# Performance work log

Hardware: AMD Instinct MI355X
Metric: run time of the kernel (lower is better)

## Reference

```python
import jax, jax.numpy as jnp
import numpy as np

MACRO_CURVE_ORDER = 3
MAX_ACTION_LEN = 24
NUM_CURVES = 8
VOCAB = 361
NUM_LAYERS = 6
HID = 32


def setup_inputs() -> dict:
    key = jax.random.key(0)
    ks = iter(jax.random.split(key, 32))
    B, N_PART, P, CTX = 4096, 100, 64, 64

    def lin(k, din, dout):
        k1, k2 = jax.random.split(k)
        s = 1.0 / np.sqrt(din)
        return (jax.random.uniform(k1, (din, dout), jnp.float32, -s, s),
                jax.random.uniform(k2, (dout,), jnp.float32, -s, s))

    fc1_w, fc1_b = lin(next(ks), P, 256)
    fc2_w, fc2_b = lin(next(ks), 256, 256)
    fc3_w, fc3_b = lin(next(ks), CTX + 256, 512)
    fc4_w, fc4_b = lin(next(ks), 512, 256)
    fc5_w, fc5_b = lin(next(ks), 256, 128)
    fc6_w, fc6_b = lin(next(ks), 128, 32)
    fc10_w, fc10_b = lin(next(ks), HID, VOCAB)

    s = 1.0 / np.sqrt(HID)
    lstm_wih = jax.random.uniform(next(ks), (NUM_LAYERS, HID, 4 * HID), jnp.float32, -s, s)
    lstm_whh = jax.random.uniform(next(ks), (NUM_LAYERS, HID, 4 * HID), jnp.float32, -s, s)
    lstm_bih = jax.random.uniform(next(ks), (NUM_LAYERS, 4 * HID), jnp.float32, -s, s)
    lstm_bhh = jax.random.uniform(next(ks), (NUM_LAYERS, 4 * HID), jnp.float32, -s, s)

    return {
        "c": jax.random.normal(next(ks), (B, CTX), jnp.float32),
        "x": jax.random.normal(next(ks), (B, N_PART * P), jnp.float32),
        "hidden": jnp.zeros((NUM_LAYERS, B, HID), jnp.float32),
        "cell": jnp.zeros((NUM_LAYERS, B, HID), jnp.float32),
        "fc1_w": fc1_w, "fc1_b": fc1_b, "fc2_w": fc2_w, "fc2_b": fc2_b,
        "fc3_w": fc3_w, "fc3_b": fc3_b, "fc4_w": fc4_w, "fc4_b": fc4_b,
        "fc5_w": fc5_w, "fc5_b": fc5_b, "fc6_w": fc6_w, "fc6_b": fc6_b,
        "lstm_wih": lstm_wih, "lstm_whh": lstm_whh,
        "lstm_bih": lstm_bih, "lstm_bhh": lstm_bhh,
        "fc10_w": fc10_w, "fc10_b": fc10_b,
        "particle_size": P,
    }


def _lstm_stack(x, h, c, wih, whh, bih, bhh):
    """One time step through 6 stacked LSTM layers (PyTorch cell math)."""
    hs, cs = [], []
    inp = x
    for l in range(NUM_LAYERS):
        gates = inp @ wih[l] + bih[l] + h[l] @ whh[l] + bhh[l]  # (B, 4*HID)
        i, f, g, o = jnp.split(gates, 4, axis=-1)
        i, f, o = jax.nn.sigmoid(i), jax.nn.sigmoid(f), jax.nn.sigmoid(o)
        g = jnp.tanh(g)
        c_new = f * c[l] + i * g
        h_new = o * jnp.tanh(c_new)
        hs.append(h_new)
        cs.append(c_new)
        inp = h_new
    return inp, jnp.stack(hs), jnp.stack(cs)


def reference(c, x, hidden, cell, fc1_w, fc1_b, fc2_w, fc2_b, fc3_w, fc3_b,
              fc4_w, fc4_b, fc5_w, fc5_b, fc6_w, fc6_b,
              lstm_wih, lstm_whh, lstm_bih, lstm_bhh, fc10_w, fc10_b,
              particle_size):
    B = x.shape[0]
    # Belief (particle) encoder with mean pooling.
    xp = x.reshape(B, -1, particle_size)
    xp = jax.nn.relu(xp @ fc1_w + fc1_b)
    xp = jax.nn.relu(xp @ fc2_w + fc2_b)
    xp = xp.mean(axis=-2)  # (B, 256)
    z = jnp.concatenate([c, xp], axis=-1)
    z = jax.nn.relu(z @ fc3_w + fc3_b)
    z = jax.nn.relu(z @ fc4_w + fc4_b)
    z = jax.nn.relu(z @ fc5_w + fc5_b)
    z = jax.nn.relu(z @ fc6_w + fc6_b)  # (B, 32)

    def step(carry, _):
        xt, h, cst = carry
        xt, h, cst = _lstm_stack(xt, h, cst, lstm_wih, lstm_whh, lstm_bih, lstm_bhh)
        logits = xt @ fc10_w + fc10_b  # (B, VOCAB)
        idx = jax.lax.top_k(logits, NUM_CURVES)[1]  # (B, NUM_CURVES)
        return (xt, h, cst), idx

    (_, _, _), idxs = jax.lax.scan(step, (z, hidden, cell), None, length=MAX_ACTION_LEN)
    # (T, B, K) -> (B, T*K)
    preds = jnp.transpose(idxs, (1, 0, 2)).reshape(B, MAX_ACTION_LEN * NUM_CURVES)
    return preds
```

## Files before the change

kernel.cpp:

```cpp
#include <hip/hip_runtime.h>
#include <math.h>

#define BATCH 4096
#define NPART 100
#define PSZ   64

__device__ __forceinline__ void fma4(float4& d, const float s, const float4 v) {
    d.x = fmaf(s, v.x, d.x); d.y = fmaf(s, v.y, d.y);
    d.z = fmaf(s, v.z, d.z); d.w = fmaf(s, v.w, d.w);
}
__device__ __forceinline__ float4 addrelu4(const float4 a, const float4 b) {
    return make_float4(fmaxf(a.x + b.x, 0.f), fmaxf(a.y + b.y, 0.f),
                       fmaxf(a.z + b.z, 0.f), fmaxf(a.w + b.w, 0.f));
}

template<int NRR, int ROWS>
__device__ __forceinline__ void enc_chunk(
    const float* __restrict__ xb, const int rbase,
    const float* __restrict__ w1c, const float* __restrict__ w2c,
    float* __restrict__ h1s, float* __restrict__ xss,
    const int tid, const int rg, const int col0,
    const float4 b1a, const float4 b1b, const float4 b2a, const float4 b2b,
    float* msum)
{
    for (int i = tid; i < ROWS * 16; i += 256) {
        const int r = i >> 4, q = (i & 15) * 4;
        *(float4*)&xss[r * 68 + q] = *(const float4*)(xb + (size_t)(rbase + r) * 64 + q);
    }
    __syncthreads();

    float4 a0[NRR], a1[NRR];
    #pragma unroll
    for (int rr = 0; rr < NRR; ++rr) {
        a0[rr] = make_float4(0.f, 0.f, 0.f, 0.f);
        a1[rr] = make_float4(0.f, 0.f, 0.f, 0.f);
    }
    #pragma unroll 2
    for (int k0 = 0; k0 < 64; k0 += 4) {
        float4 bva[4], bvb[4];
        #pragma unroll
        for (int kk = 0; kk < 4; ++kk) {
            bva[kk] = *(const float4*)(w1c + (k0 + kk) * 256);
            bvb[kk] = *(const float4*)(w1c + (k0 + kk) * 256 + 4);
        }
        #pragma unroll
        for (int rr = 0; rr < NRR; ++rr) {
            const float4 a = *(const float4*)&xss[(rg + 8 * rr) * 68 + k0];
            fma4(a0[rr], a.x, bva[0]); fma4(a0[rr], a.y, bva[1]);
            fma4(a0[rr], a.z, bva[2]); fma4(a0[rr], a.w, bva[3]);
            fma4(a1[rr], a.x, bvb[0]); fma4(a1[rr], a.y, bvb[1]);
            fma4(a1[rr], a.z, bvb[2]); fma4(a1[rr], a.w, bvb[3]);
        }
    }
    #pragma unroll
    for (int rr = 0; rr < NRR; ++rr) {
        const int r = rg + 8 * rr;
        *(float4*)&h1s[r * 260 + col0]     = addrelu4(a0[rr], b1a);
        *(float4*)&h1s[r * 260 + col0 + 4] = addrelu4(a1[rr], b1b);
    }
    __syncthreads();

    float4 c0[NRR], c1[NRR];
    #pragma unroll
    for (int rr = 0; rr < NRR; ++rr) {
        c0[rr] = make_float4(0.f, 0.f, 0.f, 0.f);
        c1[rr] = make_float4(0.f, 0.f, 0.f, 0.f);
    }
    #pragma unroll 2
    for (int k0 = 0; k0 < 256; k0 += 4) {
        float4 bva[4], bvb[4];
        #pragma unroll
        for (int kk = 0; kk < 4; ++kk) {
            bva[kk] = *(const float4*)(w2c + (k0 + kk) * 256);
            bvb[kk] = *(const float4*)(w2c + (k0 + kk) * 256 + 4);
        }
        #pragma unroll
        for (int rr = 0; rr < NRR; ++rr) {
            const float4 a = *(const float4*)&h1s[(rg + 8 * rr) * 260 + k0];
            fma4(c0[rr], a.x, bva[0]); fma4(c0[rr], a.y, bva[1]);
            fma4(c0[rr], a.z, bva[2]); fma4(c0[rr], a.w, bva[3]);
            fma4(c1[rr], a.x, bvb[0]); fma4(c1[rr], a.y, bvb[1]);
            fma4(c1[rr], a.z, bvb[2]); fma4(c1[rr], a.w, bvb[3]);
        }
    }
    #pragma unroll
    for (int rr = 0; rr < NRR; ++rr) {
        if (NRR == 4 || rg < 4) {
            msum[0] += fmaxf(c0[rr].x + b2a.x, 0.f);
            msum[1] += fmaxf(c0[rr].y + b2a.y, 0.f);
            msum[2] += fmaxf(c0[rr].z + b2a.z, 0.f);
            msum[3] += fmaxf(c0[rr].w + b2a.w, 0.f);
            msum[4] += fmaxf(c1[rr].x + b2b.x, 0.f);
            msum[5] += fmaxf(c1[rr].y + b2b.y, 0.f);
            msum[6] += fmaxf(c1[rr].z + b2b.z, 0.f);
            msum[7] += fmaxf(c1[rr].w + b2b.w, 0.f);
        }
    }
    __syncthreads();
}

__global__ __launch_bounds__(256) void k_encoder(
    const float* __restrict__ x,
    const float* __restrict__ w1, const float* __restrict__ b1,
    const float* __restrict__ w2, const float* __restrict__ b2,
    float* __restrict__ xp)
{
    __shared__ __align__(16) float h1s[32 * 260];
    __shared__ __align__(16) float xss[32 * 68];
    const int tid  = threadIdx.x;
    const int b    = blockIdx.x;
    const int lane = tid & 63;
    const int wv   = tid >> 6;
    const int cg   = lane & 7;
    const int rg   = lane >> 3;
    const int col0 = wv * 64 + cg * 8;

    const float* xb  = x + (size_t)b * (NPART * PSZ);
    const float* w1c = w1 + col0;
    const float* w2c = w2 + col0;
    const float4 b1a = *(const float4*)&b1[col0];
    const float4 b1b = *(const float4*)&b1[col0 + 4];
    const float4 b2a = *(const float4*)&b2[col0];
    const float4 b2b = *(const float4*)&b2[col0 + 4];

    float msum[8] = {0.f,0.f,0.f,0.f,0.f,0.f,0.f,0.f};

    enc_chunk<4,32>(xb,  0, w1c, w2c, h1s, xss, tid, rg, col0, b1a, b1b, b2a, b2b, msum);
    enc_chunk<4,32>(xb, 32, w1c, w2c, h1s, xss, tid, rg, col0, b1a, b1b, b2a, b2b, msum);
    enc_chunk<4,32>(xb, 64, w1c, w2c, h1s, xss, tid, rg, col0, b1a, b1b, b2a, b2b, msum);
    enc_chunk<1, 4>(xb, 96, w1c, w2c, h1s, xss, tid, rg, col0, b1a, b1b, b2a, b2b, msum);

    #pragma unroll
    for (int q = 0; q < 8; ++q) {
        msum[q] += __shfl_xor(msum[q], 8, 64);
        msum[q] += __shfl_xor(msum[q], 16, 64);
        msum[q] += __shfl_xor(msum[q], 32, 64);
    }
    if (rg == 0) {
        float4 o0 = make_float4(msum[0] / 100.f, msum[1] / 100.f,
                                msum[2] / 100.f, msum[3] / 100.f);
        float4 o1 = make_float4(msum[4] / 100.f, msum[5] / 100.f,
                                msum[6] / 100.f, msum[7] / 100.f);
        *(float4*)&xp[(size_t)b * 256 + col0]     = o0;
        *(float4*)&xp[(size_t)b * 256 + col0 + 4] = o1;
    }
}

__global__ __launch_bounds__(256) void k_mlp(
    const float* __restrict__ cin, const float* __restrict__ xp,
    const float* __restrict__ w3, const float* __restrict__ b3,
    const float* __restrict__ w4, const float* __restrict__ b4,
    const float* __restrict__ w5, const float* __restrict__ b5,
    const float* __restrict__ w6, const float* __restrict__ b6,
    float* __restrict__ z)
{
    __shared__ float in0[8][320];
    __shared__ float h3[8][512];
    __shared__ float h4[8][256];
    __shared__ float h5[8][128];
    const int tid  = threadIdx.x;
    const int row0 = blockIdx.x * 8;

    for (int i = tid; i < 8 * 16; i += 256) {
        int r = i >> 4, q = i & 15;
        *(float4*)&in0[r][q * 4] = *(const float4*)&cin[(size_t)(row0 + r) * 64 + q * 4];
    }
    for (int i = tid; i < 8 * 64; i += 256) {
        int r = i >> 6, q = i & 63;
        *(float4*)&in0[r][64 + q * 4] = *(const float4*)&xp[(size_t)(row0 + r) * 256 + q * 4];
    }
    __syncthreads();

    {
        float a0[8], a1[8];
        #pragma unroll
        for (int r = 0; r < 8; ++r) { a0[r] = 0.f; a1[r] = 0.f; }
        const int c0 = tid, c1 = tid + 256;
        for (int kq = 0; kq < 80; ++kq) {
            const int k0 = kq * 4;
            float wa0 = w3[(k0+0)*512 + c0], wa1 = w3[(k0+1)*512 + c0];
            float wa2 = w3[(k0+2)*512 + c0], wa3 = w3[(k0+3)*512 + c0];
            float wb0 = w3[(k0+0)*512 + c1], wb1 = w3[(k0+1)*512 + c1];
            float wb2 = w3[(k0+2)*512 + c1], wb3 = w3[(k0+3)*512 + c1];
            #pragma unroll
            for (int r = 0; r < 8; ++r) {
                const float4 a = *(const float4*)&in0[r][k0];
                a0[r] = fmaf(a.x, wa0, fmaf(a.y, wa1, fmaf(a.z, wa2, fmaf(a.w, wa3, a0[r]))));
                a1[r] = fmaf(a.x, wb0, fmaf(a.y, wb1, fmaf(a.z, wb2, fmaf(a.w, wb3, a1[r]))));
            }
        }
        const float bb0 = b3[c0], bb1 = b3[c1];
        #pragma unroll
        for (int r = 0; r < 8; ++r) {
            h3[r][c0] = fmaxf(a0[r] + bb0, 0.f);
            h3[r][c1] = fmaxf(a1[r] + bb1, 0.f);
        }
    }
    __syncthreads();

    {
        float ac[8];
        #pragma unroll
        for (int r = 0; r < 8; ++r) ac[r] = 0.f;
        for (int kq = 0; kq < 128; ++kq) {
            const int k0 = kq * 4;
            float w0 = w4[(k0+0)*256 + tid], w1v = w4[(k0+1)*256 + tid];
            float w2v = w4[(k0+2)*256 + tid], w3v = w4[(k0+3)*256 + tid];
            #pragma unroll
            for (int r = 0; r < 8; ++r) {
                const float4 a = *(const float4*)&h3[r][k0];
                ac[r] = fmaf(a.x, w0, fmaf(a.y, w1v, fmaf(a.z, w2v, fmaf(a.w, w3v, ac[r]))));
            }
        }
        const float bb = b4[tid];
        #pragma unroll
        for (int r = 0; r < 8; ++r) h4[r][tid] = fmaxf(ac[r] + bb, 0.f);
    }
    __syncthreads();

    {
        const int c5 = tid & 127, half = tid >> 7;
        float ac[4];
        #pragma unroll
        for (int r = 0; r < 4; ++r) ac[r] = 0.f;
        for (int kq = 0; kq < 64; ++kq) {
            const int k0 = kq * 4;
            float w0 = w5[(k0+0)*128 + c5], w1v = w5[(k0+1)*128 + c5];
            float w2v = w5[(k0+2)*128 + c5], w3v = w5[(k0+3)*128 + c5];
            #pragma unroll
            for (int r = 0; r < 4; ++r) {
                const float4 a = *(const float4*)&h4[half * 4 + r][k0];
                ac[r] = fmaf(a.x, w0, fmaf(a.y, w1v, fmaf(a.z, w2v, fmaf(a.w, w3v, ac[r]))));
            }
        }
        const float bb = b5[c5];
        #pragma unroll
        for (int r = 0; r < 4; ++r) h5[half * 4 + r][c5] = fmaxf(ac[r] + bb, 0.f);
    }
    __syncthreads();

    {
        const int c6 = tid & 31, r = tid >> 5;
        float ac = 0.f;
        for (int kq = 0; kq < 32; ++kq) {
            const int k0 = kq * 4;
            float w0 = w6[(k0+0)*32 + c6], w1v = w6[(k0+1)*32 + c6];
            float w2v = w6[(k0+2)*32 + c6], w3v = w6[(k0+3)*32 + c6];
            const float4 a = *(const float4*)&h5[r][k0];
            ac = fmaf(a.x, w0, fmaf(a.y, w1v, fmaf(a.z, w2v, fmaf(a.w, w3v, ac))));
        }
        z[(size_t)(row0 + r) * 32 + c6] = fmaxf(ac + b6[c6], 0.f);
    }
}

__global__ __launch_bounds__(256) void k_lstm(
    const float* __restrict__ z,
    const float* __restrict__ hid0, const float* __restrict__ cel0,
    const float* __restrict__ wih, const float* __restrict__ whh,
    const float* __restrict__ bih, const float* __restrict__ bhh,
    const float* __restrict__ w10, const float* __restrict__ b10,
    int* __restrict__ out)
{
    __shared__ float xs[8][32];
    __shared__ float hs[6][8][32];
    __shared__ float cs[6][8][32];
    __shared__ float gates[8][128];
    __shared__ float logits[8][361];
    const int tid  = threadIdx.x;
    const int row0 = blockIdx.x * 8;

    for (int i = tid; i < 8 * 32; i += 256) xs[0][i] = z[(size_t)row0 * 32 + i];
    for (int i = tid; i < 6 * 8 * 32; i += 256) {
        int l = i >> 8, rj = i & 255;
        (&hs[0][0][0])[i] = hid0[(size_t)l * BATCH * 32 + (size_t)row0 * 32 + rj];
        (&cs[0][0][0])[i] = cel0[(size_t)l * BATCH * 32 + (size_t)row0 * 32 + rj];
    }
    __syncthreads();

    const int g  = tid & 127, rg = tid >> 7;
    const int jc = tid & 31,  jr = tid >> 5;
    const int wv = tid >> 6,  lane = tid & 63;

    for (int t = 0; t < 24; ++t) {
        for (int l = 0; l < 6; ++l) {
            const float* inp = (l == 0) ? ((t == 0) ? &xs[0][0] : &hs[5][0][0])
                                        : &hs[l - 1][0][0];
            const float* WI = wih + (size_t)l * 32 * 128;
            const float* WH = whh + (size_t)l * 32 * 128;
            const float bsum = bih[l * 128 + g] + bhh[l * 128 + g];
            float acc[4] = {bsum, bsum, bsum, bsum};
            #pragma unroll
            for (int k = 0; k < 32; k += 4) {
                float wi0 = WI[(k+0)*128 + g], wi1 = WI[(k+1)*128 + g];
                float wi2 = WI[(k+2)*128 + g], wi3 = WI[(k+3)*128 + g];
                float wh0 = WH[(k+0)*128 + g], wh1 = WH[(k+1)*128 + g];
                float wh2 = WH[(k+2)*128 + g], wh3 = WH[(k+3)*128 + g];
                #pragma unroll
                for (int rr = 0; rr < 4; ++rr) {
                    const int r = rg * 4 + rr;
                    const float4 ai = *(const float4*)&inp[r * 32 + k];
                    const float4 ah = *(const float4*)&hs[l][r][k];
                    acc[rr] = fmaf(ai.x, wi0, acc[rr]); acc[rr] = fmaf(ai.y, wi1, acc[rr]);
                    acc[rr] = fmaf(ai.z, wi2, acc[rr]); acc[rr] = fmaf(ai.w, wi3, acc[rr]);
                    acc[rr] = fmaf(ah.x, wh0, acc[rr]); acc[rr] = fmaf(ah.y, wh1, acc[rr]);
                    acc[rr] = fmaf(ah.z, wh2, acc[rr]); acc[rr] = fmaf(ah.w, wh3, acc[rr]);
                }
            }
            #pragma unroll
            for (int rr = 0; rr < 4; ++rr) gates[rg * 4 + rr][g] = acc[rr];
            __syncthreads();

            {
                const float gi = gates[jr][jc],      gf = gates[jr][32 + jc];
                const float gg = gates[jr][64 + jc], go = gates[jr][96 + jc];
                const float i_ = 1.f / (1.f + expf(-gi));
                const float f_ = 1.f / (1.f + expf(-gf));
                const float o_ = 1.f / (1.f + expf(-go));
                const float g_ = tanhf(gg);
                const float cn = f_ * cs[l][jr][jc] + i_ * g_;
                cs[l][jr][jc] = cn;
                hs[l][jr][jc] = o_ * tanhf(cn);
            }
            __syncthreads();
        }

        #pragma unroll
        for (int pass = 0; pass < 2; ++pass) {
            const int v = tid + pass * 256;
            if (v < 361) {
                const float bb = b10[v];
                float a8[8];
                #pragma unroll
                for (int r = 0; r < 8; ++r) a8[r] = bb;
                #pragma unroll
                for (int k = 0; k < 32; k += 4) {
                    float w0 = w10[(k+0)*361 + v], w1v = w10[(k+1)*361 + v];
                    float w2v = w10[(k+2)*361 + v], w3v = w10[(k+3)*361 + v];
                    #pragma unroll
                    for (int r = 0; r < 8; ++r) {
                        const float4 a = *(const float4*)&hs[5][r][k];
                        a8[r] = fmaf(a.x, w0, fmaf(a.y, w1v, fmaf(a.z, w2v, fmaf(a.w, w3v, a8[r]))));
                    }
                }
                #pragma unroll
                for (int r = 0; r < 8; ++r) logits[r][v] = a8[r];
            }
        }
        __syncthreads();

        for (int rr = 0; rr < 2; ++rr) {
            const int r = wv * 2 + rr;
            float val[6];
            #pragma unroll
            for (int s = 0; s < 6; ++s) {
                const int v = lane + 64 * s;
                val[s] = (v < 361) ? logits[r][v] : -3.4e38f;
            }
            unsigned msk = 0x3Fu;
            const int rowg = row0 + r;
            for (int sel = 0; sel < 8; ++sel) {
                float bv = -3.4e38f; int bi = 0x7FFFFFFF;
                #pragma unroll
                for (int s = 0; s < 6; ++s) {
                    if (msk & (1u << s)) {
                        const float v2 = val[s]; const int i2 = lane + 64 * s;
                        if (v2 > bv || (v2 == bv && i2 < bi)) { bv = v2; bi = i2; }
                    }
                }
                #pragma unroll
                for (int off = 32; off >= 1; off >>= 1) {
                    const float ov = __shfl_xor(bv, off, 64);
                    const int   oi = __shfl_xor(bi, off, 64);
                    if (ov > bv || (ov == bv && oi < bi)) { bv = ov; bi = oi; }
                }
                if ((bi & 63) == lane) msk &= ~(1u << (bi >> 6));
                if (lane == 0) out[(size_t)rowg * 192 + t * 8 + sel] = bi;
            }
        }
        __syncthreads();
    }
}

extern "C" void kernel_launch(void* const* d_in, const int* in_sizes, int n_in,
                              void* d_out, int out_size, void* d_ws, size_t ws_size,
                              hipStream_t stream) {
    const float* cin  = (const float*)d_in[0];
    const float* x    = (const float*)d_in[1];
    const float* hid0 = (const float*)d_in[2];
    const float* cel0 = (const float*)d_in[3];
    const float* w1 = (const float*)d_in[4];  const float* b1 = (const float*)d_in[5];
    const float* w2 = (const float*)d_in[6];  const float* b2 = (const float*)d_in[7];
    const float* w3 = (const float*)d_in[8];  const float* b3 = (const float*)d_in[9];
    const float* w4 = (const float*)d_in[10]; const float* b4 = (const float*)d_in[11];
    const float* w5 = (const float*)d_in[12]; const float* b5 = (const float*)d_in[13];
    const float* w6 = (const float*)d_in[14]; const float* b6 = (const float*)d_in[15];
    const float* wih = (const float*)d_in[16]; const float* whh = (const float*)d_in[17];
    const float* bih = (const float*)d_in[18]; const float* bhh = (const float*)d_in[19];
    const float* w10 = (const float*)d_in[20]; const float* b10 = (const float*)d_in[21];

    float* xp = (float*)d_ws;
    float* zz = xp + (size_t)BATCH * 256;
    int*   out = (int*)d_out;

    k_encoder<<<BATCH, 256, 0, stream>>>(x, w1, b1, w2, b2, xp);
    k_mlp<<<BATCH / 8, 256, 0, stream>>>(cin, xp, w3, b3, w4, b4, w5, b5, w6, b6, zz);
    k_lstm<<<BATCH / 8, 256, 0, stream>>>(zz, hid0, cel0, wih, whh, bih, bhh, w10, b10, out);
}
```

Baseline: 2.326 ms.

## Split encoder hidden layer into halves to cut LDS and raise occupancy

```diff
diff --git a/kernel.cpp b/kernel.cpp
--- a/kernel.cpp
+++ b/kernel.cpp
@@ -17,46 +17,15 @@
 template<int NRR, int ROWS>
 __device__ __forceinline__ void enc_chunk(
     const float* __restrict__ xb, const int rbase,
-    const float* __restrict__ w1c, const float* __restrict__ w2c,
+    const float* __restrict__ w1, const float* __restrict__ b1,
+    const float* __restrict__ w2,
     float* __restrict__ h1s, float* __restrict__ xss,
-    const int tid, const int rg, const int col0,
-    const float4 b1a, const float4 b1b, const float4 b2a, const float4 b2b,
-    float* msum)
+    const int tid, const int rg, const int colw, const int col2,
+    const float4 b2a, const float4 b2b, float* msum)
 {
     for (int i = tid; i < ROWS * 16; i += 256) {
         const int r = i >> 4, q = (i & 15) * 4;
         *(float4*)&xss[r * 68 + q] = *(const float4*)(xb + (size_t)(rbase + r) * 64 + q);
-    }
-    __syncthreads();
-
-    float4 a0[NRR], a1[NRR];
-    #pragma unroll
-    for (int rr = 0; rr < NRR; ++rr) {
-        a0[rr] = make_float4(0.f, 0.f, 0.f, 0.f);
-        a1[rr] = make_float4(0.f, 0.f, 0.f, 0.f);
-    }
-    #pragma unroll 2
-    for (int k0 = 0; k0 < 64; k0 += 4) {
-        float4 bva[4], bvb[4];
-        #pragma unroll
-        for (int kk = 0; kk < 4; ++kk) {
-            bva[kk] = *(const float4*)(w1c + (k0 + kk) * 256);
-            bvb[kk] = *(const float4*)(w1c + (k0 + kk) * 256 + 4);
-        }
-        #pragma unroll
-        for (int rr = 0; rr < NRR; ++rr) {
-            const float4 a = *(const float4*)&xss[(rg + 8 * rr) * 68 + k0];
-            fma4(a0[rr], a.x, bva[0]); fma4(a0[rr], a.y, bva[1]);
-            fma4(a0[rr], a.z, bva[2]); fma4(a0[rr], a.w, bva[3]);
-            fma4(a1[rr], a.x, bvb[0]); fma4(a1[rr], a.y, bvb[1]);
-            fma4(a1[rr], a.z, bvb[2]); fma4(a1[rr], a.w, bvb[3]);
-        }
-    }
-    #pragma unroll
-    for (int rr = 0; rr < NRR; ++rr) {
-        const int r = rg + 8 * rr;
-        *(float4*)&h1s[r * 260 + col0]     = addrelu4(a0[rr], b1a);
-        *(float4*)&h1s[r * 260 + col0 + 4] = addrelu4(a1[rr], b1b);
     }
     __syncthreads();
 
@@ -66,23 +35,53 @@
         c0[rr] = make_float4(0.f, 0.f, 0.f, 0.f);
         c1[rr] = make_float4(0.f, 0.f, 0.f, 0.f);
     }
-    #pragma unroll 2
-    for (int k0 = 0; k0 < 256; k0 += 4) {
-        float4 bva[4], bvb[4];
-        #pragma unroll
-        for (int kk = 0; kk < 4; ++kk) {
-            bva[kk] = *(const float4*)(w2c + (k0 + kk) * 256);
-            bvb[kk] = *(const float4*)(w2c + (k0 + kk) * 256 + 4);
-        }
-        #pragma unroll
-        for (int rr = 0; rr < NRR; ++rr) {
-            const float4 a = *(const float4*)&h1s[(rg + 8 * rr) * 260 + k0];
-            fma4(c0[rr], a.x, bva[0]); fma4(c0[rr], a.y, bva[1]);
-            fma4(c0[rr], a.z, bva[2]); fma4(c0[rr], a.w, bva[3]);
-            fma4(c1[rr], a.x, bvb[0]); fma4(c1[rr], a.y, bvb[1]);
-            fma4(c1[rr], a.z, bvb[2]); fma4(c1[rr], a.w, bvb[3]);
-        }
-    }
+
+    #pragma unroll
+    for (int half = 0; half < 2; ++half) {
+        float4 a[NRR];
+        #pragma unroll
+        for (int rr = 0; rr < NRR; ++rr) a[rr] = make_float4(0.f, 0.f, 0.f, 0.f);
+        const float* w1c = w1 + half * 128 + colw;
+        #pragma unroll 2
+        for (int k0 = 0; k0 < 64; k0 += 4) {
+            float4 bv[4];
+            #pragma unroll
+            for (int kk = 0; kk < 4; ++kk)
+                bv[kk] = *(const float4*)(w1c + (k0 + kk) * 256);
+            #pragma unroll
+            for (int rr = 0; rr < NRR; ++rr) {
+                const float4 av = *(const float4*)&xss[(rg + 8 * rr) * 68 + k0];
+                fma4(a[rr], av.x, bv[0]); fma4(a[rr], av.y, bv[1]);
+                fma4(a[rr], av.z, bv[2]); fma4(a[rr], av.w, bv[3]);
+            }
+        }
+        const float4 b1v = *(const float4*)&b1[half * 128 + colw];
+        #pragma unroll
+        for (int rr = 0; rr < NRR; ++rr)
+            *(float4*)&h1s[(rg + 8 * rr) * 132 + colw] = addrelu4(a[rr], b1v);
+        __syncthreads();
+
+        const float* w2c = w2 + (size_t)(half * 128) * 256 + col2;
+        #pragma unroll 2
+        for (int k0 = 0; k0 < 128; k0 += 4) {
+            float4 bva[4], bvb[4];
+            #pragma unroll
+            for (int kk = 0; kk < 4; ++kk) {
+                bva[kk] = *(const float4*)(w2c + (k0 + kk) * 256);
+                bvb[kk] = *(const float4*)(w2c + (k0 + kk) * 256 + 4);
+            }
+            #pragma unroll
+            for (int rr = 0; rr < NRR; ++rr) {
+                const float4 av = *(const float4*)&h1s[(rg + 8 * rr) * 132 + k0];
+                fma4(c0[rr], av.x, bva[0]); fma4(c0[rr], av.y, bva[1]);
+                fma4(c0[rr], av.z, bva[2]); fma4(c0[rr], av.w, bva[3]);
+                fma4(c1[rr], av.x, bvb[0]); fma4(c1[rr], av.y, bvb[1]);
+                fma4(c1[rr], av.z, bvb[2]); fma4(c1[rr], av.w, bvb[3]);
+            }
+        }
+        if (half == 0) __syncthreads();
+    }
+
     #pragma unroll
     for (int rr = 0; rr < NRR; ++rr) {
         if (NRR == 4 || rg < 4) {
@@ -96,39 +95,35 @@
             msum[7] += fmaxf(c1[rr].w + b2b.w, 0.f);
         }
     }
-    __syncthreads();
-}
-
-__global__ __launch_bounds__(256) void k_encoder(
+}
+
+__global__ __launch_bounds__(256, 5) void k_encoder(
     const float* __restrict__ x,
     const float* __restrict__ w1, const float* __restrict__ b1,
     const float* __restrict__ w2, const float* __restrict__ b2,
     float* __restrict__ xp)
 {
-    __shared__ __align__(16) float h1s[32 * 260];
+    __shared__ __align__(16) float h1s[32 * 132];
     __shared__ __align__(16) float xss[32 * 68];
     const int tid  = threadIdx.x;
     const int b    = blockIdx.x;
     const int lane = tid & 63;
     const int wv   = tid >> 6;
-    const int cg   = lane & 7;
+    const int cgw  = lane & 7;
     const int rg   = lane >> 3;
-    const int col0 = wv * 64 + cg * 8;
+    const int colw = wv * 32 + cgw * 4;
+    const int col2 = wv * 64 + cgw * 8;
 
     const float* xb  = x + (size_t)b * (NPART * PSZ);
-    const float* w1c = w1 + col0;
-    const float* w2c = w2 + col0;
-    const float4 b1a = *(const float4*)&b1[col0];
-    const float4 b1b = *(const float4*)&b1[col0 + 4];
-    const float4 b2a = *(const float4*)&b2[col0];
-    const float4 b2b = *(const float4*)&b2[col0 + 4];
+    const float4 b2a = *(const float4*)&b2[col2];
+    const float4 b2b = *(const float4*)&b2[col2 + 4];
 
     float msum[8] = {0.f,0.f,0.f,0.f,0.f,0.f,0.f,0.f};
 
-    enc_chunk<4,32>(xb,  0, w1c, w2c, h1s, xss, tid, rg, col0, b1a, b1b, b2a, b2b, msum);
-    enc_chunk<4,32>(xb, 32, w1c, w2c, h1s, xss, tid, rg, col0, b1a, b1b, b2a, b2b, msum);
-    enc_chunk<4,32>(xb, 64, w1c, w2c, h1s, xss, tid, rg, col0, b1a, b1b, b2a, b2b, msum);
-    enc_chunk<1, 4>(xb, 96, w1c, w2c, h1s, xss, tid, rg, col0, b1a, b1b, b2a, b2b, msum);
+    enc_chunk<4,32>(xb,  0, w1, b1, w2, h1s, xss, tid, rg, colw, col2, b2a, b2b, msum);
+    enc_chunk<4,32>(xb, 32, w1, b1, w2, h1s, xss, tid, rg, colw, col2, b2a, b2b, msum);
+    enc_chunk<4,32>(xb, 64, w1, b1, w2, h1s, xss, tid, rg, colw, col2, b2a, b2b, msum);
+    enc_chunk<1, 4>(xb, 96, w1, b1, w2, h1s, xss, tid, rg, colw, col2, b2a, b2b, msum);
 
     #pragma unroll
     for (int q = 0; q < 8; ++q) {
@@ -141,8 +136,8 @@
                                 msum[2] / 100.f, msum[3] / 100.f);
         float4 o1 = make_float4(msum[4] / 100.f, msum[5] / 100.f,
                                 msum[6] / 100.f, msum[7] / 100.f);
-        *(float4*)&xp[(size_t)b * 256 + col0]     = o0;
-        *(float4*)&xp[(size_t)b * 256 + col0 + 4] = o1;
+        *(float4*)&xp[(size_t)b * 256 + col2]     = o0;
+        *(float4*)&xp[(size_t)b * 256 + col2 + 4] = o1;
     }
 }
 
```

After: 2.563 ms. 1.1x slower.
